# Kernel tuning notes

Hardware: AMD Instinct MI355X
Metric: run time of the kernel (lower is better)

Reference implementation:

```python
import jax, jax.numpy as jnp
import numpy as np

DEGREE = 5
A = 1.0
B = 1.0
IN_F = 1024
OUT_F = 1024
BATCH = 8192


def setup_inputs() -> dict:
    key = jax.random.key(0)
    k1, k2, k3, k4 = jax.random.split(key, 4)
    x = jax.random.normal(k1, (BATCH, IN_F), dtype=jnp.float32)
    # base_weight ~ kaiming-uniform-ish scale
    bound_w = 1.0 / np.sqrt(IN_F)
    base_weight = jax.random.uniform(k2, (OUT_F, IN_F), dtype=jnp.float32,
                                     minval=-bound_w, maxval=bound_w)
    std = 1.0 / (IN_F * np.sqrt(DEGREE + 1))
    jacobi_coeffs = std * jax.random.normal(k3, (OUT_F, IN_F, DEGREE + 1), dtype=jnp.float32)
    bias = jax.random.uniform(k4, (OUT_F,), dtype=jnp.float32, minval=-bound_w, maxval=bound_w)
    return {"x": x, "base_weight": base_weight, "jacobi_coeffs": jacobi_coeffs, "bias": bias}


def _jacobi_polynomials(x):
    # x: (batch, in_features) -> (batch, in_features, DEGREE+1)
    t = jnp.tanh(x)
    polys = [jnp.ones_like(t)]
    if DEGREE >= 1:
        polys.append(0.5 * (2.0 * (A + 1.0) * t + (A - B)))
    for k in range(2, DEGREE + 1):
        # recurrence coefficients (matching torch loop where k = written index)
        alpha_n = 2.0 * k * (k + A + B) * (2 * k + A + B - 2)
        beta_n = (2 * k + A + B - 1) * (A ** 2 - B ** 2)
        gamma_n = (2 * k + A + B - 2) * (2 * k + A + B - 1) * (2 * k + A + B)
        delta_n = 2.0 * (k + A - 1) * (k + B - 1) * (2 * k + A + B)
        Acoef = (beta_n + alpha_n * t) / gamma_n
        Bcoef = delta_n / gamma_n
        polys.append(Acoef * polys[k - 1] - Bcoef * polys[k - 2])
    return jnp.stack(polys, axis=-1)


def reference(x, base_weight, jacobi_coeffs, bias):
    # base branch: SiLU then linear
    base_out = jax.nn.silu(x) @ base_weight.T  # (b, out)
    # jacobi branch
    P = _jacobi_polynomials(x)  # (b, in, deg+1)
    jac_out = jnp.einsum('bik,oik->bo', P, jacobi_coeffs)
    return base_out + jac_out + bias
```

## Files before the change

### kernel.cpp

```cpp
#include <hip/hip_runtime.h>
#include <hip/hip_bf16.h>
#include <cstdint>
#include <cstddef>

#define BATCH   8192
#define IN_F    1024
#define OUT_F   1024
#define KAUG    (6 * 1024)
#define NSTEP   64

typedef __bf16 bf16x8 __attribute__((ext_vector_type(8)));
typedef float  f32x4  __attribute__((ext_vector_type(4)));

static constexpr size_t WAUG_B    = (size_t)OUT_F * KAUG * 2;
static constexpr size_t BIAS2_OFF = WAUG_B;

constexpr float JA[4] = {64.f/120.f, 180.f/336.f, 384.f/720.f, 700.f/1320.f};
constexpr float JB[4] = {48.f/120.f, 144.f/336.f, 320.f/720.f, 600.f/1320.f};

__device__ __forceinline__ unsigned short f2bf(float f)
{
    __hip_bfloat16 h = __float2bfloat16(f);
    return *(unsigned short*)&h;
}
__device__ __forceinline__ unsigned pack2(float lo, float hi)
{
    return (unsigned)f2bf(lo) | ((unsigned)f2bf(hi) << 16);
}
__device__ __forceinline__ unsigned cvt_pk(float lo, float hi)
{
    unsigned r;
    asm("v_cvt_pk_bf16_f32 %0, %1, %2" : "=v"(r) : "v"(lo), "v"(hi));
    return r;
}

__global__ void prep_w(const float* __restrict__ W,
                       const float* __restrict__ C,
                       const float* __restrict__ bias,
                       __hip_bfloat16* __restrict__ Waug,
                       float* __restrict__ bias2)
{
    const int o = blockIdx.x;
    const int tid = threadIdx.x;

    __shared__ __align__(16) float cs[IN_F * 6];
    __shared__ float red[4];

    const float4* C4  = (const float4*)(C + (size_t)o * IN_F * 6);
    float4*       cs4 = (float4*)cs;
#pragma unroll
    for (int k = 0; k < 6; ++k) cs4[tid + k * 256] = C4[tid + k * 256];

    const float4 wv = ((const float4*)(W + (size_t)o * IN_F))[tid];
    const float w4[4] = {wv.x, wv.y, wv.z, wv.w};

    __syncthreads();

    float f[24];
#pragma unroll
    for (int q = 0; q < 6; ++q) {
        const float4 v = cs4[tid * 6 + q];
        f[q * 4 + 0] = v.x; f[q * 4 + 1] = v.y; f[q * 4 + 2] = v.z; f[q * 4 + 3] = v.w;
    }

    unsigned pk[12];
#pragma unroll
    for (int q = 0; q < 4; ++q) {
        pk[q * 3 + 0] = pack2(w4[q],        f[q * 6 + 1]);
        pk[q * 3 + 1] = pack2(f[q * 6 + 2], f[q * 6 + 3]);
        pk[q * 3 + 2] = pack2(f[q * 6 + 4], f[q * 6 + 5]);
    }

    float s = f[0] + f[6] + f[12] + f[18];
#pragma unroll
    for (int off = 32; off > 0; off >>= 1) s += __shfl_down(s, off, 64);
    if ((tid & 63) == 0) red[tid >> 6] = s;

    __syncthreads();
    uint4* csU = (uint4*)cs;
    csU[tid * 3 + 0] = make_uint4(pk[0], pk[1], pk[2],  pk[3]);
    csU[tid * 3 + 1] = make_uint4(pk[4], pk[5], pk[6],  pk[7]);
    csU[tid * 3 + 2] = make_uint4(pk[8], pk[9], pk[10], pk[11]);
    __syncthreads();

    uint4* out4 = (uint4*)(Waug + (size_t)o * KAUG);
#pragma unroll
    for (int k = 0; k < 3; ++k) out4[tid + k * 256] = csU[tid + k * 256];

    if (tid == 0) bias2[o] = bias[o] + red[0] + red[1] + red[2] + red[3];
}

__device__ __forceinline__ void async_load16(const void* g, void* l)
{
    __builtin_amdgcn_global_load_lds(
        (const __attribute__((address_space(1))) void*)g,
        (__attribute__((address_space(3))) void*)l,
        16, 0, 0);
}

#define AS_B    24576
#define BS_B    24576
#define SMEM_B  (AS_B + 2 * BS_B)

__global__ __launch_bounds__(256, 2)
void gemm_kan(const float* __restrict__ X,
              const __hip_bfloat16* __restrict__ Waug,
              const float* __restrict__ bias2,
              float* __restrict__ out)
{
    extern __shared__ __align__(16) char smem[];

    const int tid  = threadIdx.x;
    const int lane = tid & 63;
    const int wave = tid >> 6;
    const int wm = wave & 1, wn = wave >> 1;
    const int mBase = blockIdx.x * 128;
    const int nBase = blockIdx.y * 128;

    const float* gx = X + (size_t)(mBase + (tid >> 1)) * IN_F + (tid & 1) * 8;
    char* const aw = smem + (tid >> 1) * 192 + (tid & 1) * 96;

    const __hip_bfloat16* gB[6]; int lB[6];
#pragma unroll
    for (int q = 0; q < 6; ++q) {
        const int ci = (q * 4 + wave) * 64 + lane;
        const int br = ci / 12, bc = ci - br * 12;
        gB[q] = Waug + (size_t)(nBase + br) * KAUG + bc * 8;
        lB[q] = AS_B + (q * 4 + wave) * 1024;
    }

    const int quad = lane >> 4, mr = lane & 15;
    const int aoff = (wm * 64 + mr) * 12 + quad;
    const int boff = (AS_B / 16) + (wn * 64 + mr) * 12 + quad;

    f32x4 acc[4][4] = {};

    float4 xc0 = *(const float4*)(gx);
    float4 xc1 = *(const float4*)(gx + 4);
#pragma unroll
    for (int q = 0; q < 6; ++q) async_load16(gB[q], smem + lB[q]);

#pragma unroll 1
    for (int t = 0; t < NSTEP; ++t) {
        const float xs[8] = {xc0.x, xc0.y, xc0.z, xc0.w, xc1.x, xc1.y, xc1.z, xc1.w};
        unsigned pk[24];
#pragma unroll
        for (int e = 0; e < 8; ++e) {
            const float x  = xs[e];
            const float v  = __expf(fminf(-x, 43.f));
            const float sg = __builtin_amdgcn_rcpf(1.f + v);
            const float s  = x * sg;
            const float u  = v * v;
            const float tt = (1.f - u) * __builtin_amdgcn_rcpf(1.f + u);
            const float p1 = 2.f * tt;
            const float p2 = JA[0] * tt * p1 - JB[0];
            const float p3 = JA[1] * tt * p2 - JB[1] * p1;
            const float p4 = JA[2] * tt * p3 - JB[2] * p2;
            const float p5 = JA[3] * tt * p4 - JB[3] * p3;
            pk[e * 3 + 0] = cvt_pk(s,  p1);
            pk[e * 3 + 1] = cvt_pk(p2, p3);
            pk[e * 3 + 2] = cvt_pk(p4, p5);
        }
        __syncthreads();
#pragma unroll
        for (int j = 0; j < 6; ++j)
            *(uint4*)(aw + j * 16) = make_uint4(pk[j * 4], pk[j * 4 + 1],
                                                pk[j * 4 + 2], pk[j * 4 + 3]);
        __syncthreads();

        if (t + 1 < NSTEP) {
            char* const bs = smem + ((t + 1) & 1) * BS_B;
#pragma unroll
            for (int q = 0; q < 6; ++q) async_load16(gB[q] + (t + 1) * 96, bs + lB[q]);
            xc0 = *(const float4*)(gx + (t + 1) * 16);
            xc1 = *(const float4*)(gx + (t + 1) * 16 + 4);
        }

        const bf16x8* V = (const bf16x8*)smem;
        const int bo = boff + (t & 1) * (BS_B / 16);
#pragma unroll
        for (int kc = 0; kc < 3; ++kc) {
            bf16x8 a[4], b[4];
#pragma unroll
            for (int t4 = 0; t4 < 4; ++t4) a[t4] = V[aoff + t4 * 192 + kc * 4];
#pragma unroll
            for (int t4 = 0; t4 < 4; ++t4) b[t4] = V[bo + t4 * 192 + kc * 4];
#pragma unroll
            for (int i = 0; i < 4; ++i)
#pragma unroll
                for (int jj = 0; jj < 4; ++jj)
                    acc[i][jj] = __builtin_amdgcn_mfma_f32_16x16x32_bf16(a[i], b[jj], acc[i][jj], 0, 0, 0);
        }
    }

#pragma unroll
    for (int i = 0; i < 4; ++i) {
#pragma unroll
        for (int jj = 0; jj < 4; ++jj) {
            const int col = nBase + wn * 64 + jj * 16 + mr;
            const float b2 = bias2[col];
#pragma unroll
            for (int r = 0; r < 4; ++r) {
                const int row = mBase + wm * 64 + i * 16 + quad * 4 + r;
                out[(size_t)row * OUT_F + col] = acc[i][jj][r] + b2;
            }
        }
    }
}


extern "C" void kernel_launch(void* const* d_in, const int* in_sizes, int n_in,
                              void* d_out, int out_size, void* d_ws, size_t ws_size,
                              hipStream_t stream)
{
    (void)out_size; (void)ws_size;
    const float* x    = (const float*)d_in[0];
    const float* W    = (const float*)d_in[1];
    const float* C    = (const float*)d_in[2];
    const float* bias = (const float*)d_in[3];
    for (int i = 0; i < n_in; ++i) {
        if      (in_sizes[i] == BATCH * IN_F)     x    = (const float*)d_in[i];
        else if (in_sizes[i] == OUT_F * IN_F)     W    = (const float*)d_in[i];
        else if (in_sizes[i] == OUT_F * IN_F * 6) C    = (const float*)d_in[i];
        else if (in_sizes[i] == OUT_F)            bias = (const float*)d_in[i];
    }
    float* out = (float*)d_out;
    char* ws = (char*)d_ws;
    __hip_bfloat16* Waug  = (__hip_bfloat16*)ws;
    float*          bias2 = (float*)(ws + BIAS2_OFF);

    static bool smem_attr_done = false;
    if (!smem_attr_done) {
        (void)hipFuncSetAttribute((const void*)gemm_kan,
                                  hipFuncAttributeMaxDynamicSharedMemorySize,
                                  SMEM_B);
        smem_attr_done = true;
    }

    prep_w<<<dim3(OUT_F), dim3(256), 0, stream>>>(W, C, bias, Waug, bias2);
    gemm_kan<<<dim3(BATCH / 128, OUT_F / 128), dim3(256), SMEM_B, stream>>>(
        x, Waug, bias2, out);
}
```

Before: 219.8 us.

## Double-buffer expanded A tile and stage B through registers to overlap expansion with MFMA

```diff
diff --git a/kernel.cpp b/kernel.cpp
--- a/kernel.cpp
+++ b/kernel.cpp
@@ -90,17 +90,31 @@
     if (tid == 0) bias2[o] = bias[o] + red[0] + red[1] + red[2] + red[3];
 }
 
-__device__ __forceinline__ void async_load16(const void* g, void* l)
-{
-    __builtin_amdgcn_global_load_lds(
-        (const __attribute__((address_space(1))) void*)g,
-        (__attribute__((address_space(3))) void*)l,
-        16, 0, 0);
-}
 
 #define AS_B    24576
-#define BS_B    24576
-#define SMEM_B  (AS_B + 2 * BS_B)
+#define SMEM_B  (3 * 24576)
+
+__device__ __forceinline__ void expand8r(const float4 x0, const float4 x1, unsigned* pk)
+{
+    const float xs[8] = {x0.x, x0.y, x0.z, x0.w, x1.x, x1.y, x1.z, x1.w};
+#pragma unroll
+    for (int e = 0; e < 8; ++e) {
+        const float x  = xs[e];
+        const float v  = __expf(fminf(-x, 43.f));
+        const float sg = __builtin_amdgcn_rcpf(1.f + v);
+        const float s  = x * sg;
+        const float u  = v * v;
+        const float tt = (1.f - u) * __builtin_amdgcn_rcpf(1.f + u);
+        const float p1 = 2.f * tt;
+        const float p2 = JA[0] * tt * p1 - JB[0];
+        const float p3 = JA[1] * tt * p2 - JB[1] * p1;
+        const float p4 = JA[2] * tt * p3 - JB[2] * p2;
+        const float p5 = JA[3] * tt * p4 - JB[3] * p3;
+        pk[e * 3 + 0] = cvt_pk(s,  p1);
+        pk[e * 3 + 1] = cvt_pk(p2, p3);
+        pk[e * 3 + 2] = cvt_pk(p4, p5);
+    }
+}
 
 __global__ __launch_bounds__(256, 2)
 void gemm_kan(const float* __restrict__ X,
@@ -118,79 +132,86 @@
     const int nBase = blockIdx.y * 128;
 
     const float* gx = X + (size_t)(mBase + (tid >> 1)) * IN_F + (tid & 1) * 8;
-    char* const aw = smem + (tid >> 1) * 192 + (tid & 1) * 96;
-
-    const __hip_bfloat16* gB[6]; int lB[6];
+    char* const awp = smem + (tid >> 1) * 192 + (tid & 1) * 96;
+
+    const __hip_bfloat16* gB[6];
 #pragma unroll
     for (int q = 0; q < 6; ++q) {
         const int ci = (q * 4 + wave) * 64 + lane;
         const int br = ci / 12, bc = ci - br * 12;
         gB[q] = Waug + (size_t)(nBase + br) * KAUG + bc * 8;
-        lB[q] = AS_B + (q * 4 + wave) * 1024;
-    }
+    }
+    char* const bsW = smem + 2 * AS_B + wave * 1024 + lane * 16;
 
     const int quad = lane >> 4, mr = lane & 15;
     const int aoff = (wm * 64 + mr) * 12 + quad;
-    const int boff = (AS_B / 16) + (wn * 64 + mr) * 12 + quad;
+    const int boff = 2 * (AS_B / 16) + (wn * 64 + mr) * 12 + quad;
 
     f32x4 acc[4][4] = {};
+    unsigned pk[24];
+    uint4 breg[6];
 
     float4 xc0 = *(const float4*)(gx);
     float4 xc1 = *(const float4*)(gx + 4);
 #pragma unroll
-    for (int q = 0; q < 6; ++q) async_load16(gB[q], smem + lB[q]);
+    for (int q = 0; q < 6; ++q) breg[q] = *(const uint4*)(gB[q]);
+    float4 xn0 = *(const float4*)(gx + 16);
+    float4 xn1 = *(const float4*)(gx + 20);
+
+    expand8r(xc0, xc1, pk);
+#pragma unroll
+    for (int j = 0; j < 6; ++j)
+        *(uint4*)(awp + j * 16) = make_uint4(pk[j * 4], pk[j * 4 + 1],
+                                             pk[j * 4 + 2], pk[j * 4 + 3]);
+#pragma unroll
+    for (int q = 0; q < 6; ++q) *(uint4*)(bsW + q * 4096) = breg[q];
+    __syncthreads();
+
+    const bf16x8* V = (const bf16x8*)smem;
 
 #pragma unroll 1
     for (int t = 0; t < NSTEP; ++t) {
-        const float xs[8] = {xc0.x, xc0.y, xc0.z, xc0.w, xc1.x, xc1.y, xc1.z, xc1.w};
-        unsigned pk[24];
-#pragma unroll
-        for (int e = 0; e < 8; ++e) {
-            const float x  = xs[e];
-            const float v  = __expf(fminf(-x, 43.f));
-            const float sg = __builtin_amdgcn_rcpf(1.f + v);
-            const float s  = x * sg;
-            const float u  = v * v;
-            const float tt = (1.f - u) * __builtin_amdgcn_rcpf(1.f + u);
-            const float p1 = 2.f * tt;
-            const float p2 = JA[0] * tt * p1 - JB[0];
-            const float p3 = JA[1] * tt * p2 - JB[1] * p1;
-            const float p4 = JA[2] * tt * p3 - JB[2] * p2;
-            const float p5 = JA[3] * tt * p4 - JB[3] * p3;
-            pk[e * 3 + 0] = cvt_pk(s,  p1);
-            pk[e * 3 + 1] = cvt_pk(p2, p3);
-            pk[e * 3 + 2] = cvt_pk(p4, p5);
-        }
-        __syncthreads();
-#pragma unroll
-        for (int j = 0; j < 6; ++j)
-            *(uint4*)(aw + j * 16) = make_uint4(pk[j * 4], pk[j * 4 + 1],
-                                                pk[j * 4 + 2], pk[j * 4 + 3]);
-        __syncthreads();
-
+        xc0 = xn0; xc1 = xn1;
+        if (t + 2 < NSTEP) {
+            xn0 = *(const float4*)(gx + (size_t)(t + 2) * 16);
+            xn1 = *(const float4*)(gx + (size_t)(t + 2) * 16 + 4);
+        }
         if (t + 1 < NSTEP) {
-            char* const bs = smem + ((t + 1) & 1) * BS_B;
-#pragma unroll
-            for (int q = 0; q < 6; ++q) async_load16(gB[q] + (t + 1) * 96, bs + lB[q]);
-            xc0 = *(const float4*)(gx + (t + 1) * 16);
-            xc1 = *(const float4*)(gx + (t + 1) * 16 + 4);
-        }
-
-        const bf16x8* V = (const bf16x8*)smem;
-        const int bo = boff + (t & 1) * (BS_B / 16);
+#pragma unroll
+            for (int q = 0; q < 6; ++q)
+                breg[q] = *(const uint4*)(gB[q] + (size_t)(t + 1) * 96);
+        }
+
+        const int abase = (t & 1) * (AS_B / 16) + aoff;
 #pragma unroll
         for (int kc = 0; kc < 3; ++kc) {
             bf16x8 a[4], b[4];
 #pragma unroll
-            for (int t4 = 0; t4 < 4; ++t4) a[t4] = V[aoff + t4 * 192 + kc * 4];
-#pragma unroll
-            for (int t4 = 0; t4 < 4; ++t4) b[t4] = V[bo + t4 * 192 + kc * 4];
+            for (int t4 = 0; t4 < 4; ++t4) a[t4] = V[abase + t4 * 192 + kc * 4];
+#pragma unroll
+            for (int t4 = 0; t4 < 4; ++t4) b[t4] = V[boff + t4 * 192 + kc * 4];
 #pragma unroll
             for (int i = 0; i < 4; ++i)
 #pragma unroll
                 for (int jj = 0; jj < 4; ++jj)
-                    acc[i][jj] = __builtin_amdgcn_mfma_f32_16x16x32_bf16(a[i], b[jj], acc[i][jj], 0, 0, 0);
-        }
+                    acc[i][jj] = __builtin_amdgcn_mfma_f32_16x16x32_bf16(
+                        a[i], b[jj], acc[i][jj], 0, 0, 0);
+        }
+
+        if (t + 1 < NSTEP) expand8r(xc0, xc1, pk);
+
+        __syncthreads();
+
+        if (t + 1 < NSTEP) {
+            char* const asd = awp + ((t + 1) & 1) * AS_B;
+#pragma unroll
+            for (int j = 0; j < 6; ++j)
+                *(uint4*)(asd + j * 16) = make_uint4(pk[j * 4], pk[j * 4 + 1],
+                                                     pk[j * 4 + 2], pk[j * 4 + 3]);
+#pragma unroll
+            for (int q = 0; q < 6; ++q) *(uint4*)(bsW + q * 4096) = breg[q];
+        }
+        __syncthreads();
     }
 
 #pragma unroll
```

New measurement: 369.6 us. 68.1% more time.
